# Kernel optimization log

Hardware: AMD Instinct MI355X
Metric: run time of the kernel (lower is better)

## Reference

```python
import jax, jax.numpy as jnp
import numpy as np

N, E = 50000, 400000
IN, HID, HEADS, OUT, EDIM = 128, 16, 8, 128, 32


def _lin(key, fan_in, fan_out, bias=True):
    k1, k2 = jax.random.split(key)
    s = 1.0 / np.sqrt(fan_in)
    W = jax.random.uniform(k1, (fan_in, fan_out), jnp.float32, -s, s)
    if bias:
        b = jax.random.uniform(k2, (fan_out,), jnp.float32, -s, s)
        return W, b
    return W


def setup_inputs() -> dict:
    key = jax.random.key(0)
    ks = jax.random.split(key, 16)
    x = jax.random.normal(ks[0], (N, IN), jnp.float32)
    edge_index = jax.random.randint(ks[1], (2, E), 0, N, jnp.int64)
    edge_feats = jax.random.normal(ks[2], (E, EDIM), jnp.float32)
    H1 = HEADS * HID  # 128
    Wq1, bq1 = _lin(ks[3], IN, H1)
    Wk1, bk1 = _lin(ks[4], IN, H1)
    Wv1, bv1 = _lin(ks[5], IN, H1)
    We1 = _lin(ks[6], EDIM, H1, bias=False)
    Ws1, bs1 = _lin(ks[7], IN, H1)
    Wq2, bq2 = _lin(ks[8], H1, OUT)
    Wk2, bk2 = _lin(ks[9], H1, OUT)
    Wv2, bv2 = _lin(ks[10], H1, OUT)
    We2 = _lin(ks[11], EDIM, OUT, bias=False)
    Ws2, bs2 = _lin(ks[12], H1, OUT)
    return dict(x=x, edge_index=edge_index, edge_feats=edge_feats,
                Wq1=Wq1, bq1=bq1, Wk1=Wk1, bk1=bk1, Wv1=Wv1, bv1=bv1, We1=We1, Ws1=Ws1, bs1=bs1,
                Wq2=Wq2, bq2=bq2, Wk2=Wk2, bk2=bk2, Wv2=Wv2, bv2=bv2, We2=We2, Ws2=Ws2, bs2=bs2)


def transformer_conv(x, src, dst, e, Wq, bq, Wk, bk, Wv, bv, We, Ws, bs, heads, ch, concat):
    # PyG TransformerConv: project at nodes, gather to edges.
    n = x.shape[0]
    q = (x @ Wq + bq).reshape(n, heads, ch)[dst]          # [E,H,C]
    k = (x @ Wk + bk).reshape(n, heads, ch)[src]
    v = (x @ Wv + bv).reshape(n, heads, ch)[src]
    ee = (e @ We).reshape(-1, heads, ch)                   # edge conditioning
    k = k + ee
    v = v + ee
    alpha = (q * k).sum(-1) / jnp.sqrt(jnp.asarray(ch, x.dtype))  # [E,H]
    # per-destination segment softmax
    m = jax.ops.segment_max(alpha, dst, num_segments=n)
    m = jnp.where(jnp.isfinite(m), m, 0.0)
    ea = jnp.exp(alpha - m[dst])
    denom = jax.ops.segment_sum(ea, dst, num_segments=n)
    attn = ea / jnp.maximum(denom[dst], 1e-16)
    out = jax.ops.segment_sum(attn[:, :, None] * v, dst, num_segments=n)  # [N,H,C]
    out = out.reshape(n, heads * ch) if concat else out.mean(axis=1)
    return out + x @ Ws + bs  # root_weight skip


def reference(x, edge_index, edge_feats,
              Wq1, bq1, Wk1, bk1, Wv1, bv1, We1, Ws1, bs1,
              Wq2, bq2, Wk2, bk2, Wv2, bv2, We2, Ws2, bs2):
    src, dst = edge_index[0], edge_index[1]
    h = jax.nn.relu(transformer_conv(x, src, dst, edge_feats,
                                     Wq1, bq1, Wk1, bk1, Wv1, bv1, We1, Ws1, bs1,
                                     HEADS, HID, True))
    # dropout p=0.0 (eval) -> identity
    out = jax.nn.relu(transformer_conv(h, src, dst, edge_feats,
                                       Wq2, bq2, Wk2, bk2, Wv2, bv2, We2, Ws2, bs2,
                                       1, OUT, False))
    return out
```

## Files before the change

### kernel.cpp

```cpp
#include <hip/hip_runtime.h>


using u16 = unsigned short;
using u32 = unsigned int;

#define NODES 50000
#define EDGES 400000
#define NB196 196

typedef __attribute__((ext_vector_type(8))) short bf16x8;
typedef __attribute__((ext_vector_type(4))) float f32x4;

__device__ __forceinline__ float bflo(u32 u) { return __uint_as_float(u << 16); }
__device__ __forceinline__ float bfhi(u32 u) { return __uint_as_float(u & 0xffff0000u); }
__device__ __forceinline__ u16 f2bf(float f) {
    u32 u = __float_as_uint(f);
    u += 0x7fffu + ((u >> 16) & 1u);
    return (u16)(u >> 16);
}
__device__ __forceinline__ u32 pack2(float a, float b) {
    return (u32)f2bf(a) | ((u32)f2bf(b) << 16);
}
__device__ __forceinline__ float rdv(const void* p, int i, int f) {
    return f ? ((const float*)p)[i]
             : __uint_as_float(((u32) reinterpret_cast<const u16*>(p)[i]) << 16);
}

#if __has_builtin(__builtin_amdgcn_fdot2_f32_bf16)
typedef __attribute__((ext_vector_type(2))) __bf16 bf2;
__device__ __forceinline__ float dot2bf(u32 a, u32 b, float c) {
    return __builtin_amdgcn_fdot2_f32_bf16(__builtin_bit_cast(bf2, a),
                                           __builtin_bit_cast(bf2, b), c, false);
}
#else
__device__ __forceinline__ float dot2bf(u32 a, u32 b, float c) {
    return fmaf(bflo(a), bflo(b), fmaf(bfhi(a), bfhi(b), c));
}
#endif

__device__ __forceinline__ float fexp2(float x) {
#if __has_builtin(__builtin_amdgcn_exp2f)
    return __builtin_amdgcn_exp2f(x);
#else
    return exp2f(x);
#endif
}

template <int CTRL>
__device__ __forceinline__ float dpp_addf(float x) {
    int y = __builtin_amdgcn_update_dpp(0, __float_as_int(x), CTRL, 0xF, 0xF, true);
    return x + __int_as_float(y);
}
template <int GRP>
__device__ __forceinline__ float grp_sum(float p, int lane) {
    p = dpp_addf<0xB1>(p);
    p = dpp_addf<0x4E>(p);
    p = dpp_addf<0x141>(p);
    if (GRP == 64) {
        p = dpp_addf<0x140>(p);
        p += __int_as_float(__builtin_amdgcn_ds_swizzle(__float_as_int(p), 0x401F));
        p += __int_as_float(__builtin_amdgcn_ds_bpermute((lane ^ 32) << 2,
                                                         __float_as_int(p)));
    }
    return p;
}

template <int SRC>
__device__ __forceinline__ u32 bcast8u(u32 x) {
    return (u32)__builtin_amdgcn_ds_swizzle((int)x, 0x18 | (SRC << 5));
}

__global__ __launch_bounds__(256) void fill_sentinel(float* __restrict__ out, int n, float val) {
    int i = blockIdx.x * 256 + threadIdx.x;
    if (i < n) out[i] = val;
}

__global__ __launch_bounds__(64) void detect_fmt(const u32* __restrict__ xw,
                                                 const int* __restrict__ eraw,
                                                 int* __restrict__ flags) {
    int lane = threadIdx.x;
    u32 e = (xw[lane] >> 7) & 0xffu;
    unsigned long long sane = __ballot(e >= 90u && e <= 141u);
    unsigned long long zodd = __ballot(eraw[1 + 2 * lane] == 0);
    if (lane == 0) {
        flags[0] = (sane == ~0ull) ? 0 : 1;
        flags[1] = (zodd == ~0ull) ? 1 : 0;
    }
}

#define CXB 3125
#define CDB 1563
__global__ __launch_bounds__(256) void convert_count(
    const void* __restrict__ X, const int* __restrict__ raw,
    const int* __restrict__ flags, u16* __restrict__ xbf,
    int* __restrict__ deg, int total, int E) {
    int b = blockIdx.x;
    if (b < CXB) {
        int i = (b * 256 + threadIdx.x) * 8;
        if (i >= total) return;
        if (flags[0]) {
            const float* xf = (const float*)X + i;
            float4 lo = *reinterpret_cast<const float4*>(xf);
            float4 hi = *reinterpret_cast<const float4*>(xf + 4);
            uint4 val = make_uint4(pack2(lo.x, lo.y), pack2(lo.z, lo.w),
                                   pack2(hi.x, hi.y), pack2(hi.z, hi.w));
            *reinterpret_cast<uint4*>(xbf + i) = val;
        } else {
            *reinterpret_cast<uint4*>(xbf + i) =
                *reinterpret_cast<const uint4*>((const u16*)X + i);
        }
    } else {
        int e = (b - CXB) * 256 + threadIdx.x;
        if (e < E) {
            int f = flags[1];
            int d = f ? raw[2 * (E + e)] : raw[E + e];
            if ((unsigned)d < (unsigned)NODES) atomicAdd(&deg[d], 1);
        }
    }
}

struct TPtrs {
    const void* src[8];
    u16*        dst[8];
    int         K[8];
};
struct WqeP {
    const void *Wq1, *We1, *bq1, *Wq2, *We2, *bq2;
    u16 *WtA, *WtB, *Wt2;
    float *bqe1, *bqe2;
    uint2 *WeP1, *WeP2;
};

__global__ __launch_bounds__(256) void prep_w(TPtrs P, WqeP Q, const int* __restrict__ flags) {
    int f = flags[0];
    int b = blockIdx.x;
    if (b < 32) {
        int m = b >> 2;
        int K = P.K[m];
        int quarter = (K * 128) >> 2;
        u16* d = P.dst[m];
        int base = (b & 3) * quarter;
        const float* sf = (const float*)P.src[m];
        const u16*   sb = (const u16*)P.src[m];
        for (int idx = base + threadIdx.x; idx < base + quarter; idx += 256) {
            int k = idx >> 7, n = idx & 127;
            d[n * K + k] = f ? f2bf(sf[idx]) : sb[idx];
        }
        return;
    }
    int idx = (b - 32) * 256 + threadIdx.x;
    if (idx < 32768) {
        int col = idx >> 7, i = idx & 127;
        int hh = col >> 5, d = col & 31;
        float s = 0.f;
#pragma unroll
        for (int c = 0; c < 16; ++c)
            s += rdv(Q.Wq1, i * 128 + hh * 16 + c, f) * rdv(Q.We1, d * 128 + hh * 16 + c, f);
        if (col < 128) Q.WtA[col * 128 + i] = f2bf(s);
        else           Q.WtB[(col - 128) * 128 + i] = f2bf(s);
    } else if (idx < 49152) {
        int t = idx - 32768;
        int col = t >> 7, i = t & 127;
        float s = 0.f;
        if (col < 32) {
            for (int c = 0; c < 128; ++c)
                s += rdv(Q.Wq2, i * 128 + c, f) * rdv(Q.We2, col * 128 + c, f);
        }
        Q.Wt2[col * 128 + i] = f2bf(s * 0.125f);
    } else if (idx < 49408) {
        int col = idx - 49152;
        int hh = col >> 5, d = col & 31;
        float s = 0.f;
#pragma unroll
        for (int c = 0; c < 16; ++c)
            s += rdv(Q.bq1, hh * 16 + c, f) * rdv(Q.We1, d * 128 + hh * 16 + c, f);
        Q.bqe1[col] = s;
    } else if (idx < 49536) {
        int d = idx - 49408;
        float s = 0.f;
        if (d < 32)
            for (int c = 0; c < 128; ++c)
                s += rdv(Q.bq2, c, f) * rdv(Q.We2, d * 128 + c, f);
        Q.bqe2[d] = s * 0.125f;
    } else if (idx < 50560) {
        int ent = idx - 49536;
        int t = ent >> 6, l = ent & 63, c0 = 2 * l;
        u32 xv = pack2(rdv(Q.We1, (2 * t) * 128 + c0, f),
                       rdv(Q.We1, (2 * t + 1) * 128 + c0, f));
        u32 yv = pack2(rdv(Q.We1, (2 * t) * 128 + c0 + 1, f),
                       rdv(Q.We1, (2 * t + 1) * 128 + c0 + 1, f));
        Q.WeP1[ent] = make_uint2(xv, yv);
    } else if (idx < 51584) {
        int ent = idx - 50560;
        int t = ent >> 6, l = ent & 63, c0 = 2 * l;
        u32 xv = pack2(rdv(Q.We2, (2 * t) * 128 + c0, f),
                       rdv(Q.We2, (2 * t + 1) * 128 + c0, f));
        u32 yv = pack2(rdv(Q.We2, (2 * t) * 128 + c0 + 1, f),
                       rdv(Q.We2, (2 * t + 1) * 128 + c0 + 1, f));
        Q.WeP2[ent] = make_uint2(xv, yv);
    }
}

__device__ __forceinline__ int block_scan256(int v) {
    __shared__ int ws[4];
    int t = threadIdx.x, lane = t & 63, w = t >> 6;
    int x = v;
#pragma unroll
    for (int off = 1; off < 64; off <<= 1) {
        int y = __shfl_up(x, off, 64);
        if (lane >= off) x += y;
    }
    if (lane == 63) ws[w] = x;
    __syncthreads();
#pragma unroll
    for (int j = 0; j < 3; ++j)
        if (j < w) x += ws[j];
    return x;
}

__global__ __launch_bounds__(256) void scan_a(const int* __restrict__ deg,
                                              int* __restrict__ bsum, int n) {
    int i = blockIdx.x * 256 + threadIdx.x;
    int v = (i < n) ? deg[i] : 0;
    int incl = block_scan256(v);
    if (threadIdx.x == 255) bsum[blockIdx.x] = incl;
}

__global__ __launch_bounds__(256) void scan_b(int* __restrict__ bsum, int nb) {
    int t = threadIdx.x;
    int v = (t < nb) ? bsum[t] : 0;
    int incl = block_scan256(v);
    if (t < nb) bsum[t] = incl - v;
}

__global__ __launch_bounds__(256) void scan_c(const int* __restrict__ deg,
                                              const int* __restrict__ bsum,
                                              int* __restrict__ row_ptr,
                                              int* __restrict__ cursor, int n) {
    int b = blockIdx.x;
    int i = b * 256 + threadIdx.x;
    int v = (i < n) ? deg[i] : 0;
    int incl = block_scan256(v) + bsum[b];
    if (i < n) {
        row_ptr[i + 1] = incl;
        cursor[i] = incl - v;
    }
    if (i == 0) row_ptr[0] = 0;
}

__global__ __launch_bounds__(256) void fill_csr(const int* __restrict__ raw,
                                                const int* __restrict__ flags,
                                                int* __restrict__ cursor,
                                                int* __restrict__ srcs,
                                                int* __restrict__ eids, int E) {
    int e = blockIdx.x * 256 + threadIdx.x;
    if (e < E) {
        int f = flags[1];
        int d = f ? raw[2 * (E + e)] : raw[E + e];
        int s = f ? raw[2 * e] : raw[e];
        if ((unsigned)d < (unsigned)NODES && (unsigned)s < (unsigned)NODES) {
            int pos = atomicAdd(&cursor[d], 1);
            if ((unsigned)pos < (unsigned)E) { srcs[pos] = s; eids[pos] = e; }
        }
    }
}

__global__ __launch_bounds__(256) void gather_ef(const int* __restrict__ eids,
                                                 const void* __restrict__ EF,
                                                 const int* __restrict__ flags,
                                                 u16* __restrict__ EFG, int E) {
    int t = blockIdx.x * 256 + threadIdx.x;
    int pos = t >> 2, seg = t & 3;
    if (pos >= E) return;
    int e = eids[pos];
    uint4 val;
    if (flags[0]) {
        const float* src = (const float*)EF + (size_t)e * 32 + seg * 8;
        float4 lo = *reinterpret_cast<const float4*>(src);
        float4 hi = *reinterpret_cast<const float4*>(src + 4);
        val = make_uint4(pack2(lo.x, lo.y), pack2(lo.z, lo.w),
                         pack2(hi.x, hi.y), pack2(hi.z, hi.w));
    } else {
        val = *reinterpret_cast<const uint4*>((const u16*)EF + (size_t)e * 32 + seg * 8);
    }
    *reinterpret_cast<uint4*>(EFG + (size_t)pos * 32 + seg * 8) = val;
}

struct GemmSets {
    const u16*  Wt[6];
    const void* bias[6];
    u16*        O[6];
    int         bf32[6];
    int         pitch[6];
    float       oscale[6];
};

__global__ __launch_bounds__(256) void gemm128(
    const u16* __restrict__ A, const int* __restrict__ flags, GemmSets S, int M) {
    constexpr int K = 128;
    constexpr int PAD = K + 8;
    constexpr int KV = K / 8;
    __shared__ u16 Asl[64 * PAD];
    __shared__ u16 Bsl[128 * PAD];

    const u16*  Wt   = S.Wt[blockIdx.y];
    const void* bias = S.bias[blockIdx.y];
    u16*        O    = S.O[blockIdx.y];
    int pitch = S.pitch[blockIdx.y];
    float os  = S.oscale[blockIdx.y];
    int f = S.bf32[blockIdx.y] ? 1 : flags[0];
    int m0 = blockIdx.x * 64;

    for (int idx = threadIdx.x; idx < 64 * KV; idx += 256) {
        int r = idx / KV, cv = idx % KV;
        int gr = m0 + r;
        uint4 val = make_uint4(0, 0, 0, 0);
        if (gr < M) val = *reinterpret_cast<const uint4*>(A + (size_t)gr * K + cv * 8);
        *reinterpret_cast<uint4*>(&Asl[r * PAD + cv * 8]) = val;
    }
    for (int idx = threadIdx.x; idx < 128 * KV; idx += 256) {
        int r = idx / KV, cv = idx % KV;
        *reinterpret_cast<uint4*>(&Bsl[r * PAD + cv * 8]) =
            *reinterpret_cast<const uint4*>(Wt + r * K + cv * 8);
    }
    __syncthreads();

    int lane = threadIdx.x & 63, wv = threadIdx.x >> 6;
    int l15 = lane & 15;
    int quad = lane >> 4;
    int kq = quad * 8;

    f32x4 b4[8];
#pragma unroll
    for (int nt = 0; nt < 8; ++nt) {
        int col0 = nt * 16 + quad * 4;
        if (bias) {
            if (f) {
                b4[nt] = *reinterpret_cast<const f32x4*>((const float*)bias + col0);
            } else {
                uint2 bu = *reinterpret_cast<const uint2*>((const u16*)bias + col0);
                b4[nt][0] = bflo(bu.x); b4[nt][1] = bfhi(bu.x);
                b4[nt][2] = bflo(bu.y); b4[nt][3] = bfhi(bu.y);
            }
        } else {
            b4[nt][0] = b4[nt][1] = b4[nt][2] = b4[nt][3] = 0.f;
        }
    }

    f32x4 acc[8] = {};
#pragma unroll
    for (int k0 = 0; k0 < K; k0 += 32) {
        bf16x8 xf = *reinterpret_cast<const bf16x8*>(&Asl[(wv * 16 + l15) * PAD + k0 + kq]);
#pragma unroll
        for (int nt = 0; nt < 8; ++nt) {
            bf16x8 wf = *reinterpret_cast<const bf16x8*>(&Bsl[(nt * 16 + l15) * PAD + k0 + kq]);
            acc[nt] = __builtin_amdgcn_mfma_f32_16x16x32_bf16(wf, xf, acc[nt], 0, 0, 0);
        }
    }

    int row = m0 + wv * 16 + l15;
    if (row < M) {
        u16* Orow = O + (size_t)row * pitch;
#pragma unroll
        for (int nt = 0; nt < 8; ++nt) {
            uint2 pk;
            pk.x = pack2((acc[nt][0] + b4[nt][0]) * os, (acc[nt][1] + b4[nt][1]) * os);
            pk.y = pack2((acc[nt][2] + b4[nt][2]) * os, (acc[nt][3] + b4[nt][3]) * os);
            *reinterpret_cast<uint2*>(Orow + nt * 16 + quad * 4) = pk;
        }
    }
}

template <int HEADS, int F32OUT>
__global__ __launch_bounds__(256) void attn_kernel(
    const int* __restrict__ row_ptr, const int* __restrict__ srcs,
    const u16* __restrict__ Q, const u16* __restrict__ KV,
    const u16* __restrict__ EFG,
    const u16* __restrict__ QWA, const u16* __restrict__ QWB,
    const u16* __restrict__ SK, const uint2* __restrict__ WeP,
    void* __restrict__ OUT, int nn) {
    int wv = threadIdx.x >> 6, lane = threadIdx.x & 63;
    int node = blockIdx.x * 4 + wv;
    if (node >= nn) return;
    int h = lane >> 3, j = lane & 7;
    int c0 = lane * 2;
    constexpr int GRP = (HEADS == 8) ? 8 : 64;

    u32 qb = *reinterpret_cast<const u32*>(Q + (size_t)node * 128 + c0);
    const u16* qp = (HEADS == 8)
        ? ((h < 4 ? QWA : QWB) + (size_t)node * 128 + (h & 3) * 32 + j * 4)
        : (QWA + (size_t)node * 128 + j * 4);
    uint2 qwu = *reinterpret_cast<const uint2*>(qp);

    int beg = __builtin_amdgcn_readfirstlane(row_ptr[node]);
    int end = __builtin_amdgcn_readfirstlane(row_ptr[node + 1]);

    float l_run = 0.f, a0 = 0.f, a1 = 0.f;
    float f0 = 0.f, f1 = 0.f, f2 = 0.f, f3 = 0.f;

    auto edge_step = [&](u32 kbv, u32 vbv, uint2 ebv, bool valid) {
        float p = dot2bf(qb, kbv,
                 dot2bf(qwu.x, ebv.x,
                 dot2bf(qwu.y, ebv.y, 0.f)));
        p = grp_sum<GRP>(p, lane);
        float w = fexp2(p);
        if (!valid) w = 0.f;
        l_run += w;
        a0 = fmaf(w, bflo(vbv), a0);
        a1 = fmaf(w, bfhi(vbv), a1);
        f0 = fmaf(w, bflo(ebv.x), f0); f1 = fmaf(w, bfhi(ebv.x), f1);
        f2 = fmaf(w, bflo(ebv.y), f2); f3 = fmaf(w, bfhi(ebv.y), f3);
    };

    int i = beg;
    for (; i + 8 <= end; i += 8) {
        u32 kb[8], vb[8]; uint2 eb[8];
#pragma unroll
        for (int t = 0; t < 8; ++t) {
            int s = srcs[i + t];
            const u16* kp = KV + (size_t)s * 256;
            kb[t] = *reinterpret_cast<const u32*>(kp + c0);
            vb[t] = *reinterpret_cast<const u32*>(kp + 128 + c0);
            eb[t] = *reinterpret_cast<const uint2*>(EFG + (size_t)(i + t) * 32 + j * 4);
        }
#pragma unroll
        for (int t = 0; t < 8; ++t) edge_step(kb[t], vb[t], eb[t], true);
    }
    for (; i < end; i += 4) {
        int kleft = end - i;
        u32 kb[4], vb[4]; uint2 eb[4];
#pragma unroll
        for (int t = 0; t < 4; ++t) {
            int idx = (i + t < end) ? i + t : end - 1;
            int s = srcs[idx];
            const u16* kp = KV + (size_t)s * 256;
            kb[t] = *reinterpret_cast<const u32*>(kp + c0);
            vb[t] = *reinterpret_cast<const u32*>(kp + 128 + c0);
            eb[t] = *reinterpret_cast<const uint2*>(EFG + (size_t)idx * 32 + j * 4);
        }
#pragma unroll
        for (int t = 0; t < 4; ++t) edge_step(kb[t], vb[t], eb[t], t < kleft);
    }

    u32 Fp0 = pack2(f0, f1), Fp1 = pack2(f2, f3);
    float acc0 = 0.f, acc1 = 0.f;
#define EPI(SRC) do { \
        u32 A = bcast8u<SRC>(Fp0), B = bcast8u<SRC>(Fp1); \
        uint2 w0 = WeP[(2 * SRC) * 64 + lane]; \
        uint2 w1 = WeP[(2 * SRC + 1) * 64 + lane]; \
        acc0 = dot2bf(A, w0.x, acc0); acc0 = dot2bf(B, w1.x, acc0); \
        acc1 = dot2bf(A, w0.y, acc1); acc1 = dot2bf(B, w1.y, acc1); \
    } while (0)
    EPI(0); EPI(1); EPI(2); EPI(3); EPI(4); EPI(5); EPI(6); EPI(7);
#undef EPI

    float inv = 1.f / fmaxf(l_run, 1e-16f);
    u32 sb = *reinterpret_cast<const u32*>(SK + (size_t)node * 128 + c0);
    float o0 = fmaxf(fmaf(a0 + acc0, inv, bflo(sb)), 0.f);
    float o1 = fmaxf(fmaf(a1 + acc1, inv, bfhi(sb)), 0.f);
    if (F32OUT) {
        *reinterpret_cast<float2*>((float*)OUT + (size_t)node * 128 + c0) =
            make_float2(o0, o1);
    } else {
        *reinterpret_cast<u32*>((u16*)OUT + (size_t)node * 128 + c0) = pack2(o0, o1);
    }
}

extern "C" void kernel_launch(void* const* d_in, const int* in_sizes, int n_in,
                              void* d_out, int out_size, void* d_ws, size_t ws_size,
                              hipStream_t stream) {
    const int N = NODES, E = EDGES;
    const void* x  = d_in[0];
    const int*  ei = (const int*)d_in[1];
    const void* ef = d_in[2];
    const void* Wq1 = d_in[3];  const void* bq1 = d_in[4];
    const void* Wk1 = d_in[5];  const void* bk1 = d_in[6];
    const void* Wv1 = d_in[7];  const void* bv1 = d_in[8];
    const void* We1 = d_in[9];
    const void* Ws1 = d_in[10]; const void* bs1 = d_in[11];
    const void* Wq2 = d_in[12]; const void* bq2 = d_in[13];
    const void* Wk2 = d_in[14]; const void* bk2 = d_in[15];
    const void* Wv2 = d_in[16]; const void* bv2 = d_in[17];
    const void* We2 = d_in[18];
    const void* Ws2 = d_in[19]; const void* bs2 = d_in[20];

    char* ws = (char*)d_ws;
    size_t off = 0;
    auto carve = [&](size_t bytes) -> void* {
        void* p = ws + off;
        off += (bytes + 255) & ~(size_t)255;
        return p;
    };

    u16* WtQ1 = (u16*)carve(128 * 128 * 2);
    u16* WtK1 = (u16*)carve(128 * 128 * 2);
    u16* WtV1 = (u16*)carve(128 * 128 * 2);
    u16* WtS1 = (u16*)carve(128 * 128 * 2);
    u16* WtQ2 = (u16*)carve(128 * 128 * 2);
    u16* WtK2 = (u16*)carve(128 * 128 * 2);
    u16* WtV2 = (u16*)carve(128 * 128 * 2);
    u16* WtS2 = (u16*)carve(128 * 128 * 2);
    u16* WtqA = (u16*)carve(128 * 128 * 2);
    u16* WtqB = (u16*)carve(128 * 128 * 2);
    u16* Wtq2 = (u16*)carve(128 * 128 * 2);
    float* bqe1 = (float*)carve(256 * 4);
    float* bqe2 = (float*)carve(128 * 4);
    uint2* WeP1 = (uint2*)carve(1024 * 8);
    uint2* WeP2 = (uint2*)carve(1024 * 8);
    int* flags   = (int*)carve(256);
    int* deg     = (int*)carve((size_t)N * 4);
    int* bsum    = (int*)carve((size_t)NB196 * 4);
    int* row_ptr = (int*)carve((size_t)(N + 1) * 4);
    int* cursor  = (int*)carve((size_t)N * 4);
    int* srcs    = (int*)carve((size_t)E * 4);
    int* eids    = (int*)carve((size_t)E * 4);
    u16* xbf  = (u16*)carve((size_t)N * 128 * 2);
    u16* q    = (u16*)carve((size_t)N * 128 * 2);
    u16* kv   = (u16*)carve((size_t)N * 256 * 2);
    u16* sk   = (u16*)carve((size_t)N * 128 * 2);
    u16* h    = (u16*)carve((size_t)N * 128 * 2);
    u16* qweA = (u16*)carve((size_t)N * 128 * 2);
    u16* qweB = (u16*)carve((size_t)N * 128 * 2);
    u16* qwe2 = (u16*)carve((size_t)N * 128 * 2);
    u16* efg  = (u16*)carve((size_t)E * 32 * 2);
    const size_t REQ = off;

    if (ws_size < REQ) {
        hipLaunchKernelGGL(fill_sentinel, dim3((out_size + 255) / 256), dim3(256), 0, stream,
                           (float*)d_out, out_size, 16.0f * (float)(ws_size >> 20));
        return;
    }

    const float s2_1 = 0.25f * 1.44269504f;
    const float s2_2 = 0.08838834764831845f * 1.44269504f;

    hipLaunchKernelGGL(detect_fmt, dim3(1), dim3(64), 0, stream, (const u32*)x, ei, flags);

    (void)hipMemsetAsync(deg, 0, (size_t)N * 4, stream);
    hipLaunchKernelGGL(convert_count, dim3(CXB + CDB), dim3(256), 0, stream,
                       x, ei, flags, xbf, deg, N * 128, E);

    TPtrs tp;
    tp.src[0] = Wq1; tp.dst[0] = WtQ1; tp.K[0] = 128;
    tp.src[1] = Wk1; tp.dst[1] = WtK1; tp.K[1] = 128;
    tp.src[2] = Wv1; tp.dst[2] = WtV1; tp.K[2] = 128;
    tp.src[3] = Ws1; tp.dst[3] = WtS1; tp.K[3] = 128;
    tp.src[4] = Wq2; tp.dst[4] = WtQ2; tp.K[4] = 128;
    tp.src[5] = Wk2; tp.dst[5] = WtK2; tp.K[5] = 128;
    tp.src[6] = Wv2; tp.dst[6] = WtV2; tp.K[6] = 128;
    tp.src[7] = Ws2; tp.dst[7] = WtS2; tp.K[7] = 128;
    WqeP wp;
    wp.Wq1 = Wq1; wp.We1 = We1; wp.bq1 = bq1;
    wp.Wq2 = Wq2; wp.We2 = We2; wp.bq2 = bq2;
    wp.WtA = WtqA; wp.WtB = WtqB; wp.Wt2 = Wtq2;
    wp.bqe1 = bqe1; wp.bqe2 = bqe2;
    wp.WeP1 = WeP1; wp.WeP2 = WeP2;
    hipLaunchKernelGGL(prep_w, dim3(32 + 202), dim3(256), 0, stream, tp, wp, flags);

    hipLaunchKernelGGL(scan_a, dim3(NB196), dim3(256), 0, stream, deg, bsum, N);
    hipLaunchKernelGGL(scan_b, dim3(1), dim3(256), 0, stream, bsum, NB196);
    hipLaunchKernelGGL(scan_c, dim3(NB196), dim3(256), 0, stream, deg, bsum, row_ptr, cursor, N);
    hipLaunchKernelGGL(fill_csr, dim3((E + 255) / 256), dim3(256), 0, stream, ei, flags, cursor,
                       srcs, eids, E);

    hipLaunchKernelGGL(gather_ef, dim3(E * 4 / 256), dim3(256), 0, stream,
                       eids, ef, flags, efg, E);

    const int gN = (N + 63) / 64;
    const int gA = (N + 3) / 4;

    {
        GemmSets S;
        S.Wt[0] = WtQ1; S.bias[0] = bq1;  S.O[0] = q;        S.bf32[0] = 0; S.pitch[0] = 128; S.oscale[0] = s2_1;
        S.Wt[1] = WtK1; S.bias[1] = bk1;  S.O[1] = kv;       S.bf32[1] = 0; S.pitch[1] = 256; S.oscale[1] = 1.f;
        S.Wt[2] = WtV1; S.bias[2] = bv1;  S.O[2] = kv + 128; S.bf32[2] = 0; S.pitch[2] = 256; S.oscale[2] = 1.f;
        S.Wt[3] = WtS1; S.bias[3] = bs1;  S.O[3] = sk;       S.bf32[3] = 0; S.pitch[3] = 128; S.oscale[3] = 1.f;
        S.Wt[4] = WtqA; S.bias[4] = bqe1;       S.O[4] = qweA; S.bf32[4] = 1; S.pitch[4] = 128; S.oscale[4] = s2_1;
        S.Wt[5] = WtqB; S.bias[5] = bqe1 + 128; S.O[5] = qweB; S.bf32[5] = 1; S.pitch[5] = 128; S.oscale[5] = s2_1;
        hipLaunchKernelGGL(gemm128, dim3(gN, 6), dim3(256), 0, stream, xbf, flags, S, N);
    }
    hipLaunchKernelGGL((attn_kernel<8, 0>), dim3(gA), dim3(256), 0, stream,
                       row_ptr, srcs, q, kv, efg, qweA, qweB, sk, WeP1, (void*)h, N);

    {
        GemmSets S;
        S.Wt[0] = WtQ2; S.bias[0] = bq2;  S.O[0] = q;        S.bf32[0] = 0; S.pitch[0] = 128; S.oscale[0] = s2_2;
        S.Wt[1] = WtK2; S.bias[1] = bk2;  S.O[1] = kv;       S.bf32[1] = 0; S.pitch[1] = 256; S.oscale[1] = 1.f;
        S.Wt[2] = WtV2; S.bias[2] = bv2;  S.O[2] = kv + 128; S.bf32[2] = 0; S.pitch[2] = 256; S.oscale[2] = 1.f;
        S.Wt[3] = WtS2; S.bias[3] = bs2;  S.O[3] = sk;       S.bf32[3] = 0; S.pitch[3] = 128; S.oscale[3] = 1.f;
        S.Wt[4] = Wtq2; S.bias[4] = bqe2; S.O[4] = qwe2;     S.bf32[4] = 1; S.pitch[4] = 128; S.oscale[4] = s2_2;
        S.Wt[5] = Wtq2; S.bias[5] = bqe2; S.O[5] = qwe2;     S.bf32[5] = 1; S.pitch[5] = 128; S.oscale[5] = s2_2;
        hipLaunchKernelGGL(gemm128, dim3(gN, 5), dim3(256), 0, stream, h, flags, S, N);
    }
    hipLaunchKernelGGL((attn_kernel<1, 1>), dim3(gA), dim3(256), 0, stream,
                       row_ptr, srcs, q, kv, efg, qwe2, qwe2, sk, WeP2, d_out, N);
}
```

Measured before the change: 429.8 us.

## Loop weight sets inside GEMM block to reuse the loaded A tile

The multi-output GEMM previously launched one block per (row tile, weight set) and reloaded the same 64-row activation tile for every set. Each block now loads its A tile into shared memory once and loops over all weight sets, reloading only the weight tile between barriers. This cuts global reads of A by a factor of the set count but shrinks the grid by that factor (782 blocks instead of several thousand) and serializes the per-set work within a block. prep_w is also refactored with the transpose dimension K hard-coded to 128.

```diff
diff --git a/kernel.cpp b/kernel.cpp
--- a/kernel.cpp
+++ b/kernel.cpp
@@ -131,24 +131,7 @@
     uint2 *WeP1, *WeP2;
 };
 
-__global__ __launch_bounds__(256) void prep_w(TPtrs P, WqeP Q, const int* __restrict__ flags) {
-    int f = flags[0];
-    int b = blockIdx.x;
-    if (b < 32) {
-        int m = b >> 2;
-        int K = P.K[m];
-        int quarter = (K * 128) >> 2;
-        u16* d = P.dst[m];
-        int base = (b & 3) * quarter;
-        const float* sf = (const float*)P.src[m];
-        const u16*   sb = (const u16*)P.src[m];
-        for (int idx = base + threadIdx.x; idx < base + quarter; idx += 256) {
-            int k = idx >> 7, n = idx & 127;
-            d[n * K + k] = f ? f2bf(sf[idx]) : sb[idx];
-        }
-        return;
-    }
-    int idx = (b - 32) * 256 + threadIdx.x;
+__device__ __forceinline__ void wqe_item(const WqeP& Q, int idx, int f) {
     if (idx < 32768) {
         int col = idx >> 7, i = idx & 127;
         int hh = col >> 5, d = col & 31;
@@ -201,6 +184,26 @@
     }
 }
 
+__global__ __launch_bounds__(256) void prep_w(TPtrs P, WqeP Q, const int* __restrict__ flags) {
+    int f = flags[0];
+    int b = blockIdx.x;
+    if (b < 32) {
+        int m = b >> 2;
+        int quarter = 16384 >> 2;
+        u16* d = P.dst[m];
+        int base = (b & 3) * quarter;
+        const float* sf = (const float*)P.src[m];
+        const u16*   sb = (const u16*)P.src[m];
+        for (int idx = base + threadIdx.x; idx < base + quarter; idx += 256) {
+            int k = idx >> 7, n = idx & 127;
+            d[n * 128 + k] = f ? f2bf(sf[idx]) : sb[idx];
+        }
+        return;
+    }
+    int idx = (b - 32) * 256 + threadIdx.x;
+    if (idx < 51584) wqe_item(Q, idx, f);
+}
+
 __device__ __forceinline__ int block_scan256(int v) {
     __shared__ int ws[4];
     int t = threadIdx.x, lane = t & 63, w = t >> 6;
@@ -295,20 +298,16 @@
     float       oscale[6];
 };
 
-__global__ __launch_bounds__(256) void gemm128(
-    const u16* __restrict__ A, const int* __restrict__ flags, GemmSets S, int M) {
+__global__ __launch_bounds__(256) void gemm128m(
+    const u16* __restrict__ A, const int* __restrict__ flags, GemmSets S,
+    int nsets, int M) {
     constexpr int K = 128;
     constexpr int PAD = K + 8;
     constexpr int KV = K / 8;
     __shared__ u16 Asl[64 * PAD];
     __shared__ u16 Bsl[128 * PAD];
 
-    const u16*  Wt   = S.Wt[blockIdx.y];
-    const void* bias = S.bias[blockIdx.y];
-    u16*        O    = S.O[blockIdx.y];
-    int pitch = S.pitch[blockIdx.y];
-    float os  = S.oscale[blockIdx.y];
-    int f = S.bf32[blockIdx.y] ? 1 : flags[0];
+    int fin = flags[0];
     int m0 = blockIdx.x * 64;
 
     for (int idx = threadIdx.x; idx < 64 * KV; idx += 256) {
@@ -318,55 +317,66 @@
         if (gr < M) val = *reinterpret_cast<const uint4*>(A + (size_t)gr * K + cv * 8);
         *reinterpret_cast<uint4*>(&Asl[r * PAD + cv * 8]) = val;
     }
-    for (int idx = threadIdx.x; idx < 128 * KV; idx += 256) {
-        int r = idx / KV, cv = idx % KV;
-        *reinterpret_cast<uint4*>(&Bsl[r * PAD + cv * 8]) =
-            *reinterpret_cast<const uint4*>(Wt + r * K + cv * 8);
-    }
-    __syncthreads();
 
     int lane = threadIdx.x & 63, wv = threadIdx.x >> 6;
     int l15 = lane & 15;
     int quad = lane >> 4;
     int kq = quad * 8;
-
-    f32x4 b4[8];
-#pragma unroll
-    for (int nt = 0; nt < 8; ++nt) {
-        int col0 = nt * 16 + quad * 4;
-        if (bias) {
-            if (f) {
-                b4[nt] = *reinterpret_cast<const f32x4*>((const float*)bias + col0);
+    int row = m0 + wv * 16 + l15;
+
+    for (int si = 0; si < nsets; ++si) {
+        const u16*  Wt   = S.Wt[si];
+        const void* bias = S.bias[si];
+        u16*        O    = S.O[si];
+        int   pitch = S.pitch[si];
+        float os    = S.oscale[si];
+        int   f     = S.bf32[si] ? 1 : fin;
+
+        __syncthreads();
+        for (int idx = threadIdx.x; idx < 128 * KV; idx += 256) {
+            int r = idx / KV, cv = idx % KV;
+            *reinterpret_cast<uint4*>(&Bsl[r * PAD + cv * 8]) =
+                *reinterpret_cast<const uint4*>(Wt + r * K + cv * 8);
+        }
+        __syncthreads();
+
+        f32x4 b4[8];
+#pragma unroll
+        for (int nt = 0; nt < 8; ++nt) {
+            int col0 = nt * 16 + quad * 4;
+            if (bias) {
+                if (f) {
+                    b4[nt] = *reinterpret_cast<const f32x4*>((const float*)bias + col0);
+                } else {
+                    uint2 bu = *reinterpret_cast<const uint2*>((const u16*)bias + col0);
+                    b4[nt][0] = bflo(bu.x); b4[nt][1] = bfhi(bu.x);
+                    b4[nt][2] = bflo(bu.y); b4[nt][3] = bfhi(bu.y);
+                }
             } else {
-                uint2 bu = *reinterpret_cast<const uint2*>((const u16*)bias + col0);
-                b4[nt][0] = bflo(bu.x); b4[nt][1] = bfhi(bu.x);
-                b4[nt][2] = bflo(bu.y); b4[nt][3] = bfhi(bu.y);
+                b4[nt][0] = b4[nt][1] = b4[nt][2] = b4[nt][3] = 0.f;
             }
-        } else {
-            b4[nt][0] = b4[nt][1] = b4[nt][2] = b4[nt][3] = 0.f;
-        }
-    }
-
-    f32x4 acc[8] = {};
-#pragma unroll
-    for (int k0 = 0; k0 < K; k0 += 32) {
-        bf16x8 xf = *reinterpret_cast<const bf16x8*>(&Asl[(wv * 16 + l15) * PAD + k0 + kq]);
-#pragma unroll
-        for (int nt = 0; nt < 8; ++nt) {
-            bf16x8 wf = *reinterpret_cast<const bf16x8*>(&Bsl[(nt * 16 + l15) * PAD + k0 + kq]);
-            acc[nt] = __builtin_amdgcn_mfma_f32_16x16x32_bf16(wf, xf, acc[nt], 0, 0, 0);
-        }
-    }
-
-    int row = m0 + wv * 16 + l15;
-    if (row < M) {
-        u16* Orow = O + (size_t)row * pitch;
-#pragma unroll
-        for (int nt = 0; nt < 8; ++nt) {
-            uint2 pk;
-            pk.x = pack2((acc[nt][0] + b4[nt][0]) * os, (acc[nt][1] + b4[nt][1]) * os);
-            pk.y = pack2((acc[nt][2] + b4[nt][2]) * os, (acc[nt][3] + b4[nt][3]) * os);
-            *reinterpret_cast<uint2*>(Orow + nt * 16 + quad * 4) = pk;
+        }
+
+        f32x4 acc[8] = {};
+#pragma unroll
+        for (int k0 = 0; k0 < K; k0 += 32) {
+            bf16x8 xf = *reinterpret_cast<const bf16x8*>(&Asl[(wv * 16 + l15) * PAD + k0 + kq]);
+#pragma unroll
+            for (int nt = 0; nt < 8; ++nt) {
+                bf16x8 wf = *reinterpret_cast<const bf16x8*>(&Bsl[(nt * 16 + l15) * PAD + k0 + kq]);
+                acc[nt] = __builtin_amdgcn_mfma_f32_16x16x32_bf16(wf, xf, acc[nt], 0, 0, 0);
+            }
+        }
+
+        if (row < M) {
+            u16* Orow = O + (size_t)row * pitch;
+#pragma unroll
+            for (int nt = 0; nt < 8; ++nt) {
+                uint2 pk;
+                pk.x = pack2((acc[nt][0] + b4[nt][0]) * os, (acc[nt][1] + b4[nt][1]) * os);
+                pk.y = pack2((acc[nt][2] + b4[nt][2]) * os, (acc[nt][3] + b4[nt][3]) * os);
+                *reinterpret_cast<uint2*>(Orow + nt * 16 + quad * 4) = pk;
+            }
         }
     }
 }
@@ -577,7 +587,7 @@
         S.Wt[3] = WtS1; S.bias[3] = bs1;  S.O[3] = sk;       S.bf32[3] = 0; S.pitch[3] = 128; S.oscale[3] = 1.f;
         S.Wt[4] = WtqA; S.bias[4] = bqe1;       S.O[4] = qweA; S.bf32[4] = 1; S.pitch[4] = 128; S.oscale[4] = s2_1;
         S.Wt[5] = WtqB; S.bias[5] = bqe1 + 128; S.O[5] = qweB; S.bf32[5] = 1; S.pitch[5] = 128; S.oscale[5] = s2_1;
-        hipLaunchKernelGGL(gemm128, dim3(gN, 6), dim3(256), 0, stream, xbf, flags, S, N);
+        hipLaunchKernelGGL(gemm128m, dim3(gN), dim3(256), 0, stream, xbf, flags, S, 6, N);
     }
     hipLaunchKernelGGL((attn_kernel<8, 0>), dim3(gA), dim3(256), 0, stream,
                        row_ptr, srcs, q, kv, efg, qweA, qweB, sk, WeP1, (void*)h, N);
@@ -590,7 +600,7 @@
         S.Wt[3] = WtS2; S.bias[3] = bs2;  S.O[3] = sk;       S.bf32[3] = 0; S.pitch[3] = 128; S.oscale[3] = 1.f;
         S.Wt[4] = Wtq2; S.bias[4] = bqe2; S.O[4] = qwe2;     S.bf32[4] = 1; S.pitch[4] = 128; S.oscale[4] = s2_2;
         S.Wt[5] = Wtq2; S.bias[5] = bqe2; S.O[5] = qwe2;     S.bf32[5] = 1; S.pitch[5] = 128; S.oscale[5] = s2_2;
-        hipLaunchKernelGGL(gemm128, dim3(gN, 5), dim3(256), 0, stream, h, flags, S, N);
+        hipLaunchKernelGGL(gemm128m, dim3(gN), dim3(256), 0, stream, h, flags, S, 5, N);
     }
     hipLaunchKernelGGL((attn_kernel<1, 1>), dim3(gA), dim3(256), 0, stream,
                        row_ptr, srcs, q, kv, efg, qwe2, qwe2, sk, WeP2, d_out, N);
```

After: 431.0 us. Within noise of the previous version (+0.3%).
